# Performance work log

Hardware: AMD Instinct MI355X
Metric: run time of the kernel (lower is better)

## Reference

```python
import jax, jax.numpy as jnp
import numpy as np


def setup_inputs() -> dict:
    key = jax.random.key(0)
    k1, k2 = jax.random.split(key)
    N, D = 65536, 256
    X = jax.random.normal(k1, (N, D), dtype=jnp.float32)
    X_hat = jax.random.normal(k2, (N, D), dtype=jnp.float32)
    return {"X": X, "X_hat": X_hat}


def reference(X, X_hat):
    # X, X_hat: [N, D]
    N = X.shape[0]
    # Original sorts X_hat per dim, then for each sorted value counts how many
    # x[j] <= xhat[i] via an O(N^2) broadcast. Since counting <= against a set
    # is order-free in x, sorting x and using searchsorted(side='right') gives
    # the identical count in O(N log N).
    xhat = jnp.sort(X_hat, axis=0)          # [N, D]
    xs = jnp.sort(X, axis=0)                # [N, D]
    counts = jax.vmap(
        lambda a, v: jnp.searchsorted(a, v, side='right'),
        in_axes=1, out_axes=1,
    )(xs, xhat)                              # [N, D] int, == sum(xhat[i] >= x)
    u = (counts.astype(jnp.float32) + 1.0) / jnp.float32(N + 2)  # [N, D]
    # AD weights (2i - 1), i = 1..N
    coef = (2.0 * jnp.arange(1, N + 1, dtype=jnp.float32) - 1.0)[:, None]  # [N,1]
    w = -jnp.mean(coef * (jnp.log(u) + jnp.log1p(-jnp.flip(u, axis=0))), axis=0)  # [D]
    dist = jnp.mean(w - jnp.float32(N))      # scalar: mean over dims of (w_d - N)
    return dist
```

## Files before the change

### kernel.cpp

```cpp
#include <hip/hip_runtime.h>
#include <stdint.h>
#include <math.h>

#define NR 65536
#define NRH 32768
#define NC 256

__device__ __forceinline__ uint32_t f2key(float f) {
  uint32_t b = __float_as_uint(f);
  return (b & 0x80000000u) ? ~b : (b | 0x80000000u);
}

__global__ __launch_bounds__(256) void k_transpose_key(const float* __restrict__ X,
                                                       const float* __restrict__ Xh,
                                                       uint32_t* __restrict__ outX,
                                                       uint32_t* __restrict__ outH) {
  __shared__ uint32_t tile[64][260];
  const float* in = blockIdx.z ? Xh : X;
  uint32_t* out = blockIdx.z ? outH : outX;
  const int t = threadIdx.x;
  const int r0 = blockIdx.x * 64;
#pragma unroll
  for (int i = 0; i < 16; ++i) {
    int row = i * 4 + (t >> 6);
    const float4* rp = (const float4*)(in + (size_t)(r0 + row) * NC);
    float4 v = rp[t & 63];
    uint4 k4;
    k4.x = f2key(v.x); k4.y = f2key(v.y); k4.z = f2key(v.z); k4.w = f2key(v.w);
    *(uint4*)&tile[row][(t & 63) * 4] = k4;
  }
  __syncthreads();
  const int c0 = t >> 3;
  const int rb = 4 * (t & 7);
#pragma unroll
  for (int cc = 0; cc < 8; ++cc) {
    int c = cc * 32 + c0;
#pragma unroll
    for (int h = 0; h < 2; ++h) {
      int r = 32 * h + rb;
      uint4 o;
      o.x = tile[r][c]; o.y = tile[r + 1][c];
      o.z = tile[r + 2][c]; o.w = tile[r + 3][c];
      *(uint4*)(out + (size_t)c * NR + r0 + r) = o;
    }
  }
}

__global__ __launch_bounds__(1024) void k_allhist(const uint32_t* __restrict__ kX,
                                                  const uint32_t* __restrict__ kH,
                                                  uint32_t* __restrict__ FH,
                                                  uint32_t* __restrict__ HZ,
                                                  uint32_t* __restrict__ HH,
                                                  float2* __restrict__ tab) {
  const int bid = blockIdx.x, t = threadIdx.x;
  if (bid >= 512) {
    int v = (bid - 512) * 256 + (t & 255);
    if (t < 256 && v <= 65536) {
      float2 p;
      p.x = (float)log((double)(v + 1));
      p.y = (float)log((double)(65537 - v));
      tab[v] = p;
    }
    return;
  }
  __shared__ uint32_t h12[8][2][256];
  __shared__ uint32_t h3[16][256];
  __shared__ uint32_t hz[2][256];
  const int arr = bid >> 8, col = bid & 255;
  const uint32_t* src = (arr ? kH : kX) + (size_t)col * NR;
  for (int i = t; i < 8 * 2 * 256; i += 1024) ((uint32_t*)h12)[i] = 0;
  for (int i = t; i < 16 * 256; i += 1024) ((uint32_t*)h3)[i] = 0;
  if (t < 512) ((uint32_t*)hz)[t] = 0;
  if (t < 256) {
    size_t sl = ((size_t)arr * 256 + col) * 256 + t;
#pragma unroll
    for (int p = 0; p < 2; ++p) HH[(size_t)p * 2 * 65536 + sl] = 0;
  }
  __syncthreads();
  const int cp = t >> 7;
  const int cp16 = t >> 6;
  const uint4* s4 = (const uint4*)src;
  for (int i = t; i < NR / 4; i += 1024) {
    uint4 v = s4[i];
    const bool inH0 = i < (NRH / 4);
    uint32_t a[4] = {v.x, v.y, v.z, v.w};
#pragma unroll
    for (int e = 0; e < 4; ++e) {
      uint32_t x = a[e];
      atomicAdd(&h12[cp][0][(x >> 8) & 255u], 1u);
      atomicAdd(&h12[cp][1][(x >> 16) & 255u], 1u);
      atomicAdd(&h3[cp16][x >> 24], 1u);
      if (inH0) atomicAdd(&hz[cp & 1][(x >> 8) & 255u], 1u);
    }
  }
  __syncthreads();
  if (t < 256) {
    size_t sl = ((size_t)arr * 256 + col) * 256 + t;
#pragma unroll
    for (int p = 0; p < 2; ++p) {
      uint32_t s = 0;
#pragma unroll
      for (int c = 0; c < 8; ++c) s += h12[c][p][t];
      FH[(size_t)p * 2 * 65536 + sl] = s;
    }
    uint32_t s3 = 0;
#pragma unroll
    for (int c = 0; c < 16; ++c) s3 += h3[c][t];
    FH[(size_t)2 * 2 * 65536 + sl] = s3;
    HZ[sl] = hz[0][t] + hz[1][t];
  }
}

__global__ __launch_bounds__(512, 8) void k_radix_pass(
    const uint32_t* __restrict__ s0, uint32_t* __restrict__ d0,
    const uint32_t* __restrict__ s1, uint32_t* __restrict__ d1, int shift,
    const uint32_t* __restrict__ FHp, const uint32_t* __restrict__ HINp,
    uint32_t* __restrict__ HOUTp) {
  const int bid = blockIdx.x;
  const int arr = bid >> 9, col = (bid >> 1) & 255, half = bid & 1;
  const uint32_t* src = (arr ? s1 : s0) + (size_t)col * NR + (size_t)half * NRH;
  uint32_t* dst = (arr ? d1 : d0) + (size_t)col * NR;
  const size_t sl = ((size_t)arr * 256 + col) * 256;
  const uint32_t* fh = FHp + sl;
  const uint32_t* hin = HINp + sl;
  uint32_t* hout = HOUTp ? HOUTp + sl : (uint32_t*)0;

  __shared__ uint32_t waveCnt[8][256];
  __shared__ uint32_t stageP[2][2048];
  __shared__ uint32_t runoff[3][256];
  __shared__ uint32_t chunkStartP[2][256];
  __shared__ uint32_t chunkTot[256];
  __shared__ uint32_t nh[4][256];

  const int t = threadIdx.x;
  const int lane = t & 63, w = t >> 6;
  const uint64_t ltm = (1ULL << lane) - 1ULL;

  for (int i = t; i < 4 * 256; i += 512) ((uint32_t*)nh)[i] = 0;
  if (t < 256) runoff[0][t] = fh[t];
  __syncthreads();
  if (w == 0) {
    uint32_t carry = 0;
#pragma unroll
    for (int q = 0; q < 4; ++q) {
      int d = lane + 64 * q;
      uint32_t v = runoff[0][d];
      uint32_t inc = v;
      for (int off = 1; off < 64; off <<= 1) {
        uint32_t nn = __shfl_up(inc, off);
        if (lane >= off) inc += nn;
      }
      runoff[0][d] = carry + inc - v + (half ? hin[d] : 0u);
      carry += __shfl(inc, 63);
    }
  }
  __syncthreads();

  const int NCH = NRH / 2048;
  uint32_t key[4];
#pragma unroll
  for (int k = 0; k < 4; ++k) key[k] = src[256 * w + 64 * k + lane];

  for (int r = 0; r < NCH; ++r) {
    const int sp = r & 1;
    const int rp = r % 3;
    const int cb = r * 2048;
#pragma unroll
    for (int z = 0; z < 4; ++z) waveCnt[w][lane + 64 * z] = 0;
    __builtin_amdgcn_wave_barrier();
    uint32_t nxt[4];
    const bool more = (r + 1) < NCH;
    if (more) {
#pragma unroll
      for (int k = 0; k < 4; ++k)
        nxt[k] = src[cb + 2048 + 256 * w + 64 * k + lane];
    }
    uint32_t rnk[4];
#pragma unroll
    for (int k = 0; k < 4; ++k) {
      uint32_t d = (key[k] >> shift) & 255u;
      uint32_t pre = waveCnt[w][d];
      uint64_t m = ~0ULL;
#pragma unroll
      for (int b = 0; b < 8; ++b) {
        uint64_t bb = __ballot((d >> b) & 1u);
        m &= ((d >> b) & 1u) ? bb : ~bb;
      }
      uint32_t lower = (uint32_t)__popcll(m & ltm);
      rnk[k] = pre + lower;
      if (lower == 0) waveCnt[w][d] = pre + (uint32_t)__popcll(m);
      __builtin_amdgcn_wave_barrier();
    }
    __syncthreads();
    if (t < 256) {
      int d = t;
      uint32_t run = 0;
#pragma unroll
      for (int ww = 0; ww < 8; ++ww) {
        uint32_t tmp = waveCnt[ww][d];
        waveCnt[ww][d] = run;
        run += tmp;
      }
      runoff[rp == 2 ? 0 : rp + 1][d] = runoff[rp][d] + run;
      chunkTot[d] = run;
    }
    __syncthreads();
    if (w == 0) {
      uint32_t carry = 0;
#pragma unroll
      for (int q = 0; q < 4; ++q) {
        int d = lane + 64 * q;
        uint32_t run = chunkTot[d];
        uint32_t inc = run;
        for (int off = 1; off < 64; off <<= 1) {
          uint32_t nn = __shfl_up(inc, off);
          if (lane >= off) inc += nn;
        }
        chunkStartP[sp][d] = carry + inc - run;
        carry += __shfl(inc, 63);
      }
    }
    __syncthreads();
    if (r > 0) {
      const int psp = sp ^ 1;
      const int prp = (rp + 2) % 3;
#pragma unroll
      for (int k = 0; k < 4; ++k) {
        int p = t + 512 * k;
        uint32_t kk = stageP[psp][p];
        uint32_t d = (kk >> shift) & 255u;
        uint32_t g = runoff[prp][d] + (uint32_t)p - chunkStartP[psp][d];
        dst[g] = kk;
        if (hout && g < NRH)
          atomicAdd(&nh[w & 3][(kk >> (shift + 8)) & 255u], 1u);
      }
    }
#pragma unroll
    for (int k = 0; k < 4; ++k) {
      uint32_t d = (key[k] >> shift) & 255u;
      stageP[sp][chunkStartP[sp][d] + waveCnt[w][d] + rnk[k]] = key[k];
    }
    if (more) {
#pragma unroll
      for (int k = 0; k < 4; ++k) key[k] = nxt[k];
    }
  }
  __syncthreads();
  {
    const int psp = (NCH - 1) & 1;
    const int prp = (NCH - 1) % 3;
#pragma unroll
    for (int k = 0; k < 4; ++k) {
      int p = t + 512 * k;
      uint32_t kk = stageP[psp][p];
      uint32_t d = (kk >> shift) & 255u;
      uint32_t g = runoff[prp][d] + (uint32_t)p - chunkStartP[psp][d];
      dst[g] = kk;
      if (hout && g < NRH)
        atomicAdd(&nh[w & 3][(kk >> (shift + 8)) & 255u], 1u);
    }
  }
  if (hout) {
    __syncthreads();
    if (t < 256) {
      uint32_t s = nh[0][t] + nh[1][t] + nh[2][t] + nh[3][t];
      if (s) atomicAdd(&hout[t], s);
    }
  }
}

__global__ __launch_bounds__(1024, 8) void k_ad_accum(const uint32_t* __restrict__ xs,
                                                      const uint32_t* __restrict__ xh,
                                                      const float2* __restrict__ tab,
                                                      double* __restrict__ colsum) {
  constexpr int BCH = 4096, CAPA = 5120;
  __shared__ uint32_t ldsA[CAPA];
  __shared__ int sh_jnext;
  __shared__ double red16[16];
  const int bid = blockIdx.x, col = bid >> 2, q = bid & 3, t = threadIdx.x;
  const int lane = t & 63, w = t >> 6;
  const uint32_t* A = xs + (size_t)col * NR;
  const uint32_t* B = xh + (size_t)col * NR;
  const int base0 = q * (NR / 4);
  int jb;
  {
    uint32_t v0 = B[base0];
    int lo = 0, hi = NR;
    while (lo < hi) {
      int mid = (lo + hi) >> 1;
      if (A[mid] <= v0) lo = mid + 1; else hi = mid;
    }
    jb = lo;
  }
  double acc = 0.0;
  for (int r = 0; r < (NR / 4) / BCH; ++r) {
    const int base = base0 + r * BCH;
    const uint4 bv = *(const uint4*)(B + base + 4 * t);
    const int jb0 = jb & ~3;
    const int avail = min(CAPA, NR - jb0);
    const uint4* a4 = (const uint4*)(A + jb0);
    for (int i = t; i < avail / 4; i += 1024) ((uint4*)ldsA)[i] = a4[i];
    __syncthreads();
    uint32_t be[4] = {bv.x, bv.y, bv.z, bv.w};
    int lo = 0, hi = avail;
    while (lo < hi) {
      int mid = (lo + hi) >> 1;
      if (ldsA[mid] <= be[0]) lo = mid + 1; else hi = mid;
    }
    int j = lo;
    long jg = -1;
#pragma unroll
    for (int k = 0; k < 4; ++k) {
      uint32_t v = be[k];
      if (jg < 0) {
        while (j < avail && ldsA[j] <= v) ++j;
        if (j == avail && jb0 + avail < NR) jg = jb0 + avail;
      }
      if (jg >= 0) {
        while (jg < NR && A[jg] <= v) ++jg;
      }
      int cnt = (jg >= 0) ? (int)jg : jb0 + j;
      int i = base + 4 * t + k;
      float2 p = tab[cnt];
      acc += (double)((float)(2 * i + 1) * p.x + (float)(2 * NR - 1 - 2 * i) * p.y);
    }
    if (t == 1023) sh_jnext = (jg >= 0) ? (int)jg : jb0 + j;
    __syncthreads();
    jb = sh_jnext;
  }
  for (int off = 32; off > 0; off >>= 1) acc += __shfl_down(acc, off);
  if (lane == 0) red16[w] = acc;
  __syncthreads();
  if (t == 0) {
    double s = 0.0;
#pragma unroll
    for (int i = 0; i < 16; ++i) s += red16[i];
    colsum[bid] = s;
  }
}

__global__ __launch_bounds__(1024) void k_final(const double* __restrict__ colsum,
                                                float* __restrict__ out) {
  __shared__ double red16[16];
  int t = threadIdx.x, lane = t & 63, w = t >> 6;
  double v = colsum[t];
  for (int off = 32; off > 0; off >>= 1) v += __shfl_down(v, off);
  if (lane == 0) red16[w] = v;
  __syncthreads();
  if (t == 0) {
    double total = 0.0;
#pragma unroll
    for (int i = 0; i < 16; ++i) total += red16[i];
    double dist = -total / ((double)NR * (double)NC)
                  + 2.0 * (double)NR * log(65538.0) - (double)NR;
    out[0] = (float)dist;
  }
}

extern "C" void kernel_launch(void* const* d_in, const int* in_sizes, int n_in,
                              void* d_out, int out_size, void* d_ws, size_t ws_size,
                              hipStream_t stream) {
  const float* X = (const float*)d_in[0];
  const float* Xh = (const float*)d_in[1];
  float* out = (float*)d_out;

  const size_t NEL = (size_t)NC * NR;
  const size_t B = 65536;
  uint32_t* P0 = (uint32_t*)d_ws;
  uint32_t* P1 = P0 + NEL;
  uint32_t* P2 = P1 + NEL;

  dim3 tg(NR / 64, 1, 2);
  k_transpose_key<<<tg, 256, 0, stream>>>(X, Xh, P0, P2);

  const size_t HSP = 12 * B;
  const size_t TABW = 65537 * 2;
  uint32_t* nul = nullptr;
  bool fused = ws_size >= (4 * NEL + HSP + TABW + 2048) * sizeof(uint32_t);
  if (fused) {
    uint32_t* P3 = P2 + NEL;
    uint32_t* FH = P3 + NEL;
    uint32_t* HZ = FH + 6 * B;
    uint32_t* HH = HZ + 2 * B;
    float2* tab = (float2*)(HH + 4 * B);
    double* colsum = (double*)(tab + 65537);
    k_allhist<<<769, 1024, 0, stream>>>(P0, P2, FH, HZ, HH, tab);
    k_radix_pass<<<1024, 512, 0, stream>>>(P0, P1, P2, P3, 8,  FH,         HZ,         HH);
    k_radix_pass<<<1024, 512, 0, stream>>>(P1, P0, P3, P2, 16, FH + 2 * B, HH,         HH + 2 * B);
    k_radix_pass<<<1024, 512, 0, stream>>>(P0, P1, P2, P3, 24, FH + 4 * B, HH + 2 * B, nul);
    k_ad_accum<<<1024, 1024, 0, stream>>>(P1, P3, tab, colsum);
    k_final<<<1, 1024, 0, stream>>>(colsum, out);
  } else {
    uint32_t* FH = P2 + NEL;
    uint32_t* HZ = FH + 6 * B;
    uint32_t* HH = HZ + 2 * B;
    float2* tab = (float2*)(HH + 4 * B);
    double* colsum = (double*)(tab + 65537);
    k_allhist<<<769, 1024, 0, stream>>>(P0, P2, FH, HZ, HH, tab);
    {
      k_radix_pass<<<512, 512, 0, stream>>>(P0, P1, P0, P1, 8,  FH,         HZ,         HH);
      k_radix_pass<<<512, 512, 0, stream>>>(P1, P0, P1, P0, 16, FH + 2 * B, HH,         HH + 2 * B);
      k_radix_pass<<<512, 512, 0, stream>>>(P0, P1, P0, P1, 24, FH + 4 * B, HH + 2 * B, nul);
    }
    {
      size_t ao = B;
      k_radix_pass<<<512, 512, 0, stream>>>(P2, P0, P2, P0, 8,  FH + ao,         HZ + ao,         HH + ao);
      k_radix_pass<<<512, 512, 0, stream>>>(P0, P2, P0, P2, 16, FH + 2 * B + ao, HH + ao,         HH + 2 * B + ao);
      k_radix_pass<<<512, 512, 0, stream>>>(P2, P0, P2, P0, 24, FH + 4 * B + ao, HH + 2 * B + ao, nul);
    }
    k_ad_accum<<<1024, 1024, 0, stream>>>(P1, P0, tab, colsum);
    k_final<<<1, 1024, 0, stream>>>(colsum, out);
  }
}
```

Before: 572.5 us.

## Fuse transpose and histogram into one prep kernel, fold final reduce into accum

Merges the key transpose, the digit histograms and the log table into a single k_prep launch. The histogram blocks now read the raw row-major floats directly, each covering a 4096-row by 16-column tile, and merge partial counts into global histograms with atomics. This removes the separate pass that re-read the transposed keys. The final reduction moves into k_ad_accum through a last-block-done counter, which removes one launch. In exchange it needs two memsets, adds global atomics, and makes the histogram reads strided.

```diff
diff --git a/kernel.cpp b/kernel.cpp
--- a/kernel.cpp
+++ b/kernel.cpp
@@ -11,51 +11,50 @@
   return (b & 0x80000000u) ? ~b : (b | 0x80000000u);
 }
 
-__global__ __launch_bounds__(256) void k_transpose_key(const float* __restrict__ X,
-                                                       const float* __restrict__ Xh,
-                                                       uint32_t* __restrict__ outX,
-                                                       uint32_t* __restrict__ outH) {
-  __shared__ uint32_t tile[64][260];
-  const float* in = blockIdx.z ? Xh : X;
-  uint32_t* out = blockIdx.z ? outH : outX;
-  const int t = threadIdx.x;
-  const int r0 = blockIdx.x * 64;
-#pragma unroll
-  for (int i = 0; i < 16; ++i) {
-    int row = i * 4 + (t >> 6);
-    const float4* rp = (const float4*)(in + (size_t)(r0 + row) * NC);
-    float4 v = rp[t & 63];
-    uint4 k4;
-    k4.x = f2key(v.x); k4.y = f2key(v.y); k4.z = f2key(v.z); k4.w = f2key(v.w);
-    *(uint4*)&tile[row][(t & 63) * 4] = k4;
-  }
-  __syncthreads();
-  const int c0 = t >> 3;
-  const int rb = 4 * (t & 7);
-#pragma unroll
-  for (int cc = 0; cc < 8; ++cc) {
-    int c = cc * 32 + c0;
-#pragma unroll
-    for (int h = 0; h < 2; ++h) {
-      int r = 32 * h + rb;
-      uint4 o;
-      o.x = tile[r][c]; o.y = tile[r + 1][c];
-      o.z = tile[r + 2][c]; o.w = tile[r + 3][c];
-      *(uint4*)(out + (size_t)c * NR + r0 + r) = o;
-    }
-  }
-}
-
-__global__ __launch_bounds__(1024) void k_allhist(const uint32_t* __restrict__ kX,
-                                                  const uint32_t* __restrict__ kH,
-                                                  uint32_t* __restrict__ FH,
-                                                  uint32_t* __restrict__ HZ,
-                                                  uint32_t* __restrict__ HH,
-                                                  float2* __restrict__ tab) {
+__global__ __launch_bounds__(256) void k_prep(const float* __restrict__ X,
+                                              const float* __restrict__ Xh,
+                                              uint32_t* __restrict__ outX,
+                                              uint32_t* __restrict__ outH,
+                                              uint32_t* __restrict__ FH,
+                                              uint32_t* __restrict__ HZ,
+                                              float2* __restrict__ tab) {
+  __shared__ uint32_t smem[20480];
   const int bid = blockIdx.x, t = threadIdx.x;
-  if (bid >= 512) {
-    int v = (bid - 512) * 256 + (t & 255);
-    if (t < 256 && v <= 65536) {
+  if (bid < 2048) {
+    uint32_t (*tile)[260] = (uint32_t(*)[260])smem;
+    const int z = bid >> 10, slab = bid & 1023;
+    const float* in = z ? Xh : X;
+    uint32_t* out = z ? outH : outX;
+    const int r0 = slab * 64;
+#pragma unroll
+    for (int i = 0; i < 16; ++i) {
+      int row = i * 4 + (t >> 6);
+      const float4* rp = (const float4*)(in + (size_t)(r0 + row) * NC);
+      float4 v = rp[t & 63];
+      uint4 k4;
+      k4.x = f2key(v.x); k4.y = f2key(v.y); k4.z = f2key(v.z); k4.w = f2key(v.w);
+      *(uint4*)&tile[row][(t & 63) * 4] = k4;
+    }
+    __syncthreads();
+    const int c0 = t >> 3;
+    const int rb = 4 * (t & 7);
+#pragma unroll
+    for (int cc = 0; cc < 8; ++cc) {
+      int c = cc * 32 + c0;
+#pragma unroll
+      for (int h = 0; h < 2; ++h) {
+        int r = 32 * h + rb;
+        uint4 o;
+        o.x = tile[r][c]; o.y = tile[r + 1][c];
+        o.z = tile[r + 2][c]; o.w = tile[r + 3][c];
+        *(uint4*)(out + (size_t)c * NR + r0 + r) = o;
+      }
+    }
+    return;
+  }
+  if (bid >= 2560) {
+    int v = (bid - 2560) * 256 + t;
+    if (v <= 65536) {
       float2 p;
       p.x = (float)log((double)(v + 1));
       p.y = (float)log((double)(65537 - v));
@@ -63,51 +62,46 @@
     }
     return;
   }
-  __shared__ uint32_t h12[8][2][256];
-  __shared__ uint32_t h3[16][256];
-  __shared__ uint32_t hz[2][256];
-  const int arr = bid >> 8, col = bid & 255;
-  const uint32_t* src = (arr ? kH : kX) + (size_t)col * NR;
-  for (int i = t; i < 8 * 2 * 256; i += 1024) ((uint32_t*)h12)[i] = 0;
-  for (int i = t; i < 16 * 256; i += 1024) ((uint32_t*)h3)[i] = 0;
-  if (t < 512) ((uint32_t*)hz)[t] = 0;
-  if (t < 256) {
-    size_t sl = ((size_t)arr * 256 + col) * 256 + t;
-#pragma unroll
-    for (int p = 0; p < 2; ++p) HH[(size_t)p * 2 * 65536 + sl] = 0;
-  }
-  __syncthreads();
-  const int cp = t >> 7;
-  const int cp16 = t >> 6;
-  const uint4* s4 = (const uint4*)src;
-  for (int i = t; i < NR / 4; i += 1024) {
-    uint4 v = s4[i];
-    const bool inH0 = i < (NRH / 4);
-    uint32_t a[4] = {v.x, v.y, v.z, v.w};
+  uint32_t* h12 = smem;
+  uint32_t* h3 = smem + 8192;
+  uint32_t* hz = smem + 16384;
+  const int hb = bid - 2048;
+  const int arr = hb >> 8, rem = hb & 255;
+  const int cg = rem >> 4, rs = rem & 15;
+  const float* in = arr ? Xh : X;
+  const int c0 = cg * 16, r0 = rs * 4096;
+  for (int i = t; i < 20480; i += 256) smem[i] = 0;
+  __syncthreads();
+  for (int qi = t; qi < 16384; qi += 256) {
+    int row = r0 + (qi >> 2);
+    int cq = (qi & 3) * 4;
+    int cp3 = (qi >> 2) & 1;
+    float4 v = *(const float4*)(in + (size_t)row * NC + c0 + cq);
+    float a[4] = {v.x, v.y, v.z, v.w};
 #pragma unroll
     for (int e = 0; e < 4; ++e) {
-      uint32_t x = a[e];
-      atomicAdd(&h12[cp][0][(x >> 8) & 255u], 1u);
-      atomicAdd(&h12[cp][1][(x >> 16) & 255u], 1u);
-      atomicAdd(&h3[cp16][x >> 24], 1u);
-      if (inH0) atomicAdd(&hz[cp & 1][(x >> 8) & 255u], 1u);
-    }
-  }
-  __syncthreads();
-  if (t < 256) {
-    size_t sl = ((size_t)arr * 256 + col) * 256 + t;
-#pragma unroll
-    for (int p = 0; p < 2; ++p) {
-      uint32_t s = 0;
-#pragma unroll
-      for (int c = 0; c < 8; ++c) s += h12[c][p][t];
-      FH[(size_t)p * 2 * 65536 + sl] = s;
-    }
-    uint32_t s3 = 0;
-#pragma unroll
-    for (int c = 0; c < 16; ++c) s3 += h3[c][t];
-    FH[(size_t)2 * 2 * 65536 + sl] = s3;
-    HZ[sl] = hz[0][t] + hz[1][t];
+      uint32_t x = f2key(a[e]);
+      int c = cq + e;
+      atomicAdd(&h12[(c * 2 + 0) * 256 + ((x >> 8) & 255u)], 1u);
+      atomicAdd(&h12[(c * 2 + 1) * 256 + ((x >> 16) & 255u)], 1u);
+      atomicAdd(&h3[(c * 2 + cp3) * 256 + (x >> 24)], 1u);
+      if (rs < 8) atomicAdd(&hz[c * 256 + ((x >> 8) & 255u)], 1u);
+    }
+  }
+  __syncthreads();
+  for (int i = t; i < 4096; i += 256) {
+    int c = i >> 8, b = i & 255;
+    size_t sl = ((size_t)arr * 256 + (c0 + c)) * 256 + b;
+    uint32_t v0 = h12[(c * 2 + 0) * 256 + b];
+    uint32_t v1 = h12[(c * 2 + 1) * 256 + b];
+    uint32_t v2 = h3[(c * 2 + 0) * 256 + b] + h3[(c * 2 + 1) * 256 + b];
+    if (v0) atomicAdd(&FH[sl], v0);
+    if (v1) atomicAdd(&FH[(size_t)2 * 65536 + sl], v1);
+    if (v2) atomicAdd(&FH[(size_t)4 * 65536 + sl], v2);
+    if (rs < 8) {
+      uint32_t vz = hz[c * 256 + b];
+      if (vz) atomicAdd(&HZ[sl], vz);
+    }
   }
 }
 
@@ -272,10 +266,13 @@
 __global__ __launch_bounds__(1024, 8) void k_ad_accum(const uint32_t* __restrict__ xs,
                                                       const uint32_t* __restrict__ xh,
                                                       const float2* __restrict__ tab,
-                                                      double* __restrict__ colsum) {
+                                                      double* __restrict__ colsum,
+                                                      uint32_t* __restrict__ counter,
+                                                      float* __restrict__ out) {
   constexpr int BCH = 4096, CAPA = 5120;
   __shared__ uint32_t ldsA[CAPA];
   __shared__ int sh_jnext;
+  __shared__ int sh_last;
   __shared__ double red16[16];
   const int bid = blockIdx.x, col = bid >> 2, q = bid & 3, t = threadIdx.x;
   const int lane = t & 63, w = t >> 6;
@@ -336,24 +333,24 @@
 #pragma unroll
     for (int i = 0; i < 16; ++i) s += red16[i];
     colsum[bid] = s;
-  }
-}
-
-__global__ __launch_bounds__(1024) void k_final(const double* __restrict__ colsum,
-                                                float* __restrict__ out) {
-  __shared__ double red16[16];
-  int t = threadIdx.x, lane = t & 63, w = t >> 6;
-  double v = colsum[t];
-  for (int off = 32; off > 0; off >>= 1) v += __shfl_down(v, off);
-  if (lane == 0) red16[w] = v;
-  __syncthreads();
-  if (t == 0) {
-    double total = 0.0;
-#pragma unroll
-    for (int i = 0; i < 16; ++i) total += red16[i];
-    double dist = -total / ((double)NR * (double)NC)
-                  + 2.0 * (double)NR * log(65538.0) - (double)NR;
-    out[0] = (float)dist;
+    __threadfence();
+    sh_last = (atomicAdd(counter, 1u) == 1023u) ? 1 : 0;
+  }
+  __syncthreads();
+  if (sh_last) {
+    __threadfence();
+    double v = colsum[t];
+    for (int off = 32; off > 0; off >>= 1) v += __shfl_down(v, off);
+    if (lane == 0) red16[w] = v;
+    __syncthreads();
+    if (t == 0) {
+      double total = 0.0;
+#pragma unroll
+      for (int i = 0; i < 16; ++i) total += red16[i];
+      double dist = -total / ((double)NR * (double)NC)
+                    + 2.0 * (double)NR * log(65538.0) - (double)NR;
+      out[0] = (float)dist;
+    }
   }
 }
 
@@ -370,13 +367,10 @@
   uint32_t* P1 = P0 + NEL;
   uint32_t* P2 = P1 + NEL;
 
-  dim3 tg(NR / 64, 1, 2);
-  k_transpose_key<<<tg, 256, 0, stream>>>(X, Xh, P0, P2);
-
   const size_t HSP = 12 * B;
   const size_t TABW = 65537 * 2;
   uint32_t* nul = nullptr;
-  bool fused = ws_size >= (4 * NEL + HSP + TABW + 2048) * sizeof(uint32_t);
+  bool fused = ws_size >= (4 * NEL + HSP + TABW + 2112) * sizeof(uint32_t);
   if (fused) {
     uint32_t* P3 = P2 + NEL;
     uint32_t* FH = P3 + NEL;
@@ -384,19 +378,24 @@
     uint32_t* HH = HZ + 2 * B;
     float2* tab = (float2*)(HH + 4 * B);
     double* colsum = (double*)(tab + 65537);
-    k_allhist<<<769, 1024, 0, stream>>>(P0, P2, FH, HZ, HH, tab);
+    uint32_t* counter = (uint32_t*)(colsum + 1024);
+    hipMemsetAsync(FH, 0, 12 * B * sizeof(uint32_t), stream);
+    hipMemsetAsync(counter, 0, sizeof(uint32_t), stream);
+    k_prep<<<2817, 256, 0, stream>>>(X, Xh, P0, P2, FH, HZ, tab);
     k_radix_pass<<<1024, 512, 0, stream>>>(P0, P1, P2, P3, 8,  FH,         HZ,         HH);
     k_radix_pass<<<1024, 512, 0, stream>>>(P1, P0, P3, P2, 16, FH + 2 * B, HH,         HH + 2 * B);
     k_radix_pass<<<1024, 512, 0, stream>>>(P0, P1, P2, P3, 24, FH + 4 * B, HH + 2 * B, nul);
-    k_ad_accum<<<1024, 1024, 0, stream>>>(P1, P3, tab, colsum);
-    k_final<<<1, 1024, 0, stream>>>(colsum, out);
+    k_ad_accum<<<1024, 1024, 0, stream>>>(P1, P3, tab, colsum, counter, out);
   } else {
     uint32_t* FH = P2 + NEL;
     uint32_t* HZ = FH + 6 * B;
     uint32_t* HH = HZ + 2 * B;
     float2* tab = (float2*)(HH + 4 * B);
     double* colsum = (double*)(tab + 65537);
-    k_allhist<<<769, 1024, 0, stream>>>(P0, P2, FH, HZ, HH, tab);
+    uint32_t* counter = (uint32_t*)(colsum + 1024);
+    hipMemsetAsync(FH, 0, 12 * B * sizeof(uint32_t), stream);
+    hipMemsetAsync(counter, 0, sizeof(uint32_t), stream);
+    k_prep<<<2817, 256, 0, stream>>>(X, Xh, P0, P2, FH, HZ, tab);
     {
       k_radix_pass<<<512, 512, 0, stream>>>(P0, P1, P0, P1, 8,  FH,         HZ,         HH);
       k_radix_pass<<<512, 512, 0, stream>>>(P1, P0, P1, P0, 16, FH + 2 * B, HH,         HH + 2 * B);
@@ -408,7 +407,6 @@
       k_radix_pass<<<512, 512, 0, stream>>>(P0, P2, P0, P2, 16, FH + 2 * B + ao, HH + ao,         HH + 2 * B + ao);
       k_radix_pass<<<512, 512, 0, stream>>>(P2, P0, P2, P0, 24, FH + 4 * B + ao, HH + 2 * B + ao, nul);
     }
-    k_ad_accum<<<1024, 1024, 0, stream>>>(P1, P0, tab, colsum);
-    k_final<<<1, 1024, 0, stream>>>(colsum, out);
+    k_ad_accum<<<1024, 1024, 0, stream>>>(P1, P0, tab, colsum, counter, out);
   }
 }
```

Result: slower. 616.8 us (+7.7%).
